# Performance work log

Measured on AMD Instinct MI355X. Metric: run time of the kernel, lower is better.

The kernel has to match this reference:

```python
import jax, jax.numpy as jnp
import numpy as np


def setup_inputs() -> dict:
    key = jax.random.key(0)
    B, DP, N = 4, 3, 8192
    positions = jax.random.normal(key, (B, DP, N), dtype=jnp.float32)
    return {"positions": positions, "k": 16}


def reference(positions, k):
    # positions: [B, Dp, N] ('simple' data_format)
    # Pairwise squared Euclidean distances between all N points per batch:
    # d2[b, i, j] = ||x_i - x_j||^2 = ||x_i||^2 + ||x_j||^2 - 2 x_i . x_j
    sq = jnp.sum(positions * positions, axis=1)                     # [B, N]
    dots = jnp.einsum('bdn,bdm->bnm', positions, positions)         # [B, N, N]
    d2 = sq[:, :, None] + sq[:, None, :] - 2.0 * dots               # [B, N, N]
    # k nearest neighbors (smallest distance; includes self at distance ~0)
    neg_d, idx = jax.lax.top_k(-d2, k)                              # [B, N, K]
    # Layer transposes raw op output [B, N, K] -> [B, K, N]
    NN = jnp.transpose(idx, (0, 2, 1)).astype(jnp.int32)            # [B, K, N]
    distances = jnp.transpose(-neg_d, (0, 2, 1))                    # [B, K, N]
    return (NN, distances)
```

## Files before the change

kernel.cpp:

```cpp
#include <hip/hip_runtime.h>
#include <stdint.h>

#define NPTS 8192
#define NPAIR 4096
#define NB 4
#define KNN 16
#define RQ 2
#define CCAP 20
#define DCAP 256
#define MARGIN 1.5e-3f

typedef unsigned long long u64;
typedef unsigned int u32;
typedef unsigned short u16;
typedef float f32x2 __attribute__((ext_vector_type(2)));

__device__ __forceinline__ u32 f2ord(float f) {
    u32 b = __float_as_uint(f);
    return (b & 0x80000000u) ? ~b : (b | 0x80000000u);
}
__device__ __forceinline__ float ord2f(u32 u) {
    u32 b = (u & 0x80000000u) ? (u & 0x7fffffffu) : ~u;
    return __uint_as_float(b);
}
__device__ __forceinline__ u64 shflx64(u64 v, int m) {
    u32 lo = (u32)v, hi = (u32)(v >> 32);
    lo = __shfl_xor(lo, m, 64);
    hi = __shfl_xor(hi, m, 64);
    return ((u64)hi << 32) | lo;
}

__global__ __launch_bounds__(256) void pack_kernel(const float* __restrict__ pos,
                                                   float4* __restrict__ pos8) {
    int t = blockIdx.x * 256 + threadIdx.x;
    int b = t >> 12;
    int m = t & (NPAIR - 1);
    const float* p = pos + (size_t)b * 3 * NPTS;
    float2 x = *(const float2*)&p[2 * m];
    float2 y = *(const float2*)&p[NPTS + 2 * m];
    float2 z = *(const float2*)&p[2 * NPTS + 2 * m];
    float s0 = __fadd_rn(__fadd_rn(__fmul_rn(x.x, x.x), __fmul_rn(y.x, y.x)), __fmul_rn(z.x, z.x));
    float s1 = __fadd_rn(__fadd_rn(__fmul_rn(x.y, x.y), __fmul_rn(y.y, y.y)), __fmul_rn(z.y, z.y));
    pos8[2 * t]     = make_float4(x.x, x.y, y.x, y.y);
    pos8[2 * t + 1] = make_float4(z.x, z.y, s0, s1);
}

#define RECOMP(r, idx, d2out)                                                           \
    { int _m = (int)(idx) >> 1, _h = (int)(idx) & 1;                                    \
      float4 _a = P8[2 * _m], _c = P8[2 * _m + 1];                                      \
      float _px = _h ? _a.y : _a.x, _py = _h ? _a.w : _a.z;                             \
      float _pz = _h ? _c.y : _c.x, _pw = _h ? _c.w : _c.z;                             \
      float _dot = __fmaf_rn(qz[r], _pz, __fmaf_rn(qy[r], _py, __fmul_rn(qx[r], _px))); \
      d2out = __fsub_rn(__fadd_rn(qw[r], _pw), __fmul_rn(2.0f, _dot)); }

#define PROC(Av, Cv, mm)                                                                \
    {                                                                                   \
        f32x2 x01 = {(Av).x, (Av).y}, y01 = {(Av).z, (Av).w};                           \
        f32x2 z01 = {(Cv).x, (Cv).y}, sq01 = {(Cv).z, (Cv).w};                          \
        _Pragma("unroll")                                                               \
        for (int r = 0; r < RQ; ++r) {                                                  \
            f32x2 dot01 = __builtin_elementwise_fma(                                    \
                qzv[r], z01, __builtin_elementwise_fma(qyv[r], y01, qxv[r] * x01));     \
            f32x2 val01 = __builtin_elementwise_fma(n2v, dot01, sq01);                  \
            if (val01.x < Tm[r]) { col[wv][r][c[r]][lane] = (u16)(2 * (mm));     c[r]++; } \
            if (val01.y < Tm[r]) { col[wv][r][c[r]][lane] = (u16)(2 * (mm) + 1); c[r]++; } \
        }                                                                               \
    }

#define TRIGC()                                                                         \
    {                                                                                   \
        if (__ballot(c[0] > 16)) tighten(0);                                            \
        if (__ballot(c[1] > 16)) tighten(1);                                            \
    }

__global__ __launch_bounds__(256) void knn_kernel(const float4* __restrict__ pos8,
                                                  float* __restrict__ out) {
    __shared__ u16 col[4][RQ][CCAP][64];
    __shared__ u16 dense[4][DCAP];
    const int lane = threadIdx.x & 63;
    const int wv = threadIdx.x >> 6;
    const int rowbase = blockIdx.x * (4 * RQ) + wv * RQ;
    const int b = rowbase >> 13;
    const int ib = rowbase & (NPTS - 1);
    const float4* __restrict__ P8 = pos8 + (size_t)b * NPAIR * 2;
    const u64 below = (1ull << lane) - 1ull;

    float qx[RQ], qy[RQ], qz[RQ], qw[RQ];
    {
        int m = ib >> 1;
        float4 a = P8[2 * m], cc = P8[2 * m + 1];
        qx[0] = a.x; qy[0] = a.z; qz[0] = cc.x; qw[0] = cc.z;
        qx[1] = a.y; qy[1] = a.w; qz[1] = cc.y; qw[1] = cc.w;
    }
    f32x2 qxv[RQ], qyv[RQ], qzv[RQ];
#pragma unroll
    for (int r = 0; r < RQ; ++r) {
        qxv[r] = (f32x2){qx[r], qx[r]};
        qyv[r] = (f32x2){qy[r], qy[r]};
        qzv[r] = (f32x2){qz[r], qz[r]};
    }
    const f32x2 n2v = {-2.0f, -2.0f};

    float Tm[RQ];
    int c[RQ];

    auto rank16f = [&](float v) -> float {
#pragma unroll
        for (int k = 2; k <= 64; k <<= 1)
#pragma unroll
            for (int j = k >> 1; j >= 1; j >>= 1) {
                float o = __shfl_xor(v, j, 64);
                bool up = ((lane & k) == 0) == ((lane & j) == 0);
                v = (up ? (v < o) : (v > o)) ? v : o;
            }
        return __shfl(v, 15, 64);
    };

    auto tighten = [&](int r) {
        u32 mn = 0xFFFFFFFFu;
#pragma unroll
        for (int t = 0; t < CCAP; ++t) {
            if (t < c[r]) {
                u32 idx = (u32)col[wv][r][t][lane];
                float d2; RECOMP(r, idx, d2);
                u32 o = f2ord(d2);
                mn = o < mn ? o : mn;
            }
        }
        u32 v = mn;
#pragma unroll
        for (int k = 2; k <= 64; k <<= 1)
#pragma unroll
            for (int j = k >> 1; j >= 1; j >>= 1) {
                u32 o = (u32)__shfl_xor((int)v, j, 64);
                bool up = ((lane & k) == 0) == ((lane & j) == 0);
                v = (up ? (v < o) : (v > o)) ? v : o;
            }
        u32 ordK = (u32)__shfl((int)v, 15, 64);
        int nc = 0;
#pragma unroll
        for (int t = 0; t < CCAP; ++t) {
            if (t < c[r]) {
                u32 idx = (u32)col[wv][r][t][lane];
                float d2; RECOMP(r, idx, d2);
                if (f2ord(d2) <= ordK) { col[wv][r][nc][lane] = (u16)idx; ++nc; }
            }
        }
        c[r] = nc;
#pragma unroll 1
        for (int it = 0; it < CCAP - 16; ++it) {
            if (c[r] > 16) {
                u64 mx = 0; int mt = 0;
#pragma unroll
                for (int t = 0; t < CCAP; ++t) {
                    if (t < c[r]) {
                        u32 idx = (u32)col[wv][r][t][lane];
                        float d2; RECOMP(r, idx, d2);
                        u64 key = ((u64)f2ord(d2) << 13) | idx;
                        if (key > mx) { mx = key; mt = t; }
                    }
                }
                col[wv][r][mt][lane] = col[wv][r][c[r] - 1][lane];
                c[r] -= 1;
            }
        }
        Tm[r] = fminf(Tm[r], (ord2f(ordK) - qw[r]) + MARGIN);
    };

    {
        float4 A[4], C[4];
#pragma unroll
        for (int s = 0; s < 4; ++s) {
            int m = s * 64 + lane;
            A[s] = P8[2 * m];
            C[s] = P8[2 * m + 1];
        }
#pragma unroll
        for (int r = 0; r < RQ; ++r) {
            f32x2 vv[4];
            float mn = __uint_as_float(0x7f800000u);
#pragma unroll
            for (int s = 0; s < 4; ++s) {
                f32x2 x01 = {A[s].x, A[s].y}, y01 = {A[s].z, A[s].w};
                f32x2 z01 = {C[s].x, C[s].y}, sq01 = {C[s].z, C[s].w};
                vv[s] = __builtin_elementwise_fma(
                    n2v, __builtin_elementwise_fma(qzv[r], z01,
                         __builtin_elementwise_fma(qyv[r], y01, qxv[r] * x01)), sq01);
                mn = fminf(mn, fminf(vv[s].x, vv[s].y));
            }
            float V16 = rank16f(mn);
            Tm[r] = V16 + 2.0f * MARGIN;
            c[r] = 0;
#pragma unroll
            for (int s = 0; s < 4; ++s) {
                int m = s * 64 + lane;
                if (vv[s].x < Tm[r]) { col[wv][r][c[r]][lane] = (u16)(2 * m);     c[r]++; }
                if (vv[s].y < Tm[r]) { col[wv][r][c[r]][lane] = (u16)(2 * m + 1); c[r]++; }
            }
        }
    }

#pragma unroll 1
    for (int g = 1; g < 16; ++g) {
        TRIGC();
        int base = g * 256;
        float4 A[4], C[4];
#pragma unroll
        for (int s = 0; s < 4; ++s) {
            int m = base + s * 64 + lane;
            A[s] = P8[2 * m];
            C[s] = P8[2 * m + 1];
        }
        PROC(A[0], C[0], base + lane);
        PROC(A[1], C[1], base + 64 + lane);
        TRIGC();
        PROC(A[2], C[2], base + 128 + lane);
        PROC(A[3], C[3], base + 192 + lane);
    }

#pragma unroll
    for (int r = 0; r < RQ; ++r) {
        int sum = c[r];
#pragma unroll
        for (int s2 = 1; s2 < 64; s2 <<= 1) sum += __shfl_xor(sum, s2, 64);
        if (sum > 64) tighten(r);
        int nc = 0;
#pragma unroll 1
        for (int t = 0; t < CCAP; ++t) {
            bool valid = t < c[r];
            u64 bal = __ballot(valid);
            if (!bal) break;
            if (valid) dense[wv][nc + (int)__popcll(bal & below)] = col[wv][r][t][lane];
            nc += (int)__popcll(bal);
        }
        u64 myk = ~0ULL;
        if (nc <= 64) {
            bool valid = lane < nc;
            u32 idx = valid ? (u32)dense[wv][lane] : 0u;
            float d2; RECOMP(r, idx, d2);
            u64 v = valid ? (((u64)f2ord(d2) << 13) | idx) : ~0ULL;
#pragma unroll
            for (int k = 2; k <= 64; k <<= 1)
#pragma unroll
                for (int j = k >> 1; j >= 1; j >>= 1) {
                    u64 o = shflx64(v, j);
                    bool up = ((lane & k) == 0) == ((lane & j) == 0);
                    v = (up ? (v < o) : (v > o)) ? v : o;
                }
            myk = v;
        } else {
            u64 s4[4];
#pragma unroll
            for (int t = 0; t < 4; ++t) {
                int bi = t * 64 + lane;
                bool valid = bi < nc;
                u32 idx = valid ? (u32)dense[wv][bi] : 0u;
                float d2; RECOMP(r, idx, d2);
                s4[t] = valid ? (((u64)f2ord(d2) << 13) | idx) : ~0ULL;
            }
#pragma unroll 1
            for (int rr = 0; rr < KNN; ++rr) {
                u64 lm = s4[0];
#pragma unroll
                for (int t = 1; t < 4; ++t) lm = s4[t] < lm ? s4[t] : lm;
                u64 mm = lm;
#pragma unroll
                for (int s2 = 1; s2 < 64; s2 <<= 1) { u64 o = shflx64(mm, s2); mm = o < mm ? o : mm; }
#pragma unroll
                for (int t = 0; t < 4; ++t) s4[t] = (s4[t] == mm) ? ~0ULL : s4[t];
                if (lane == rr) myk = mm;
            }
        }
        if (lane < KNN) {
            int iq = ib + r;
            size_t o1 = (size_t)(b * KNN + lane) * NPTS + iq;
            out[o1] = (float)(u32)(myk & (u64)(NPTS - 1));
            out[(size_t)NB * KNN * NPTS + o1] = ord2f((u32)(myk >> 13));
        }
    }
}

extern "C" void kernel_launch(void* const* d_in, const int* in_sizes, int n_in,
                              void* d_out, int out_size, void* d_ws, size_t ws_size,
                              hipStream_t stream) {
    const float* pos = (const float*)d_in[0];
    float* out = (float*)d_out;
    float4* pos8 = (float4*)d_ws;

    pack_kernel<<<dim3(NB * NPAIR / 256), dim3(256), 0, stream>>>(pos, pos8);
    knn_kernel<<<dim3(NB * NPTS / 8), dim3(256), 0, stream>>>(pos8, out);
}
```

Measured before the change: 184.1 us.

## Track candidate point pairs instead of single points with branchless append

Candidate lists now store the index of a point pair (the packed float4 pair) and admit a pair when the smaller of its two distances is under the threshold. Appends become branchless: the slot is always written and the counter increments conditionally. Tighten and the final selection recompute both distances of each pair, and the final sort thresholds are halved to match. This removes divergent branches in the hot scan loop, but each pair carries a possibly useless second point, so lists fill faster and tighten may run more often.

```diff
diff --git a/kernel.cpp b/kernel.cpp
--- a/kernel.cpp
+++ b/kernel.cpp
@@ -45,13 +45,12 @@
     pos8[2 * t + 1] = make_float4(z.x, z.y, s0, s1);
 }
 
-#define RECOMP(r, idx, d2out)                                                           \
-    { int _m = (int)(idx) >> 1, _h = (int)(idx) & 1;                                    \
-      float4 _a = P8[2 * _m], _c = P8[2 * _m + 1];                                      \
-      float _px = _h ? _a.y : _a.x, _py = _h ? _a.w : _a.z;                             \
-      float _pz = _h ? _c.y : _c.x, _pw = _h ? _c.w : _c.z;                             \
-      float _dot = __fmaf_rn(qz[r], _pz, __fmaf_rn(qy[r], _py, __fmul_rn(qx[r], _px))); \
-      d2out = __fsub_rn(__fadd_rn(qw[r], _pw), __fmul_rn(2.0f, _dot)); }
+#define RECOMP2(r, m, d0, d1)                                                           \
+    { float4 _a = P8[2 * (m)], _c = P8[2 * (m) + 1];                                    \
+      float _dot0 = __fmaf_rn(qz[r], _c.x, __fmaf_rn(qy[r], _a.z, __fmul_rn(qx[r], _a.x))); \
+      float _dot1 = __fmaf_rn(qz[r], _c.y, __fmaf_rn(qy[r], _a.w, __fmul_rn(qx[r], _a.y))); \
+      d0 = __fsub_rn(__fadd_rn(qw[r], _c.z), __fmul_rn(2.0f, _dot0));                   \
+      d1 = __fsub_rn(__fadd_rn(qw[r], _c.w), __fmul_rn(2.0f, _dot1)); }
 
 #define PROC(Av, Cv, mm)                                                                \
     {                                                                                   \
@@ -62,8 +61,8 @@
             f32x2 dot01 = __builtin_elementwise_fma(                                    \
                 qzv[r], z01, __builtin_elementwise_fma(qyv[r], y01, qxv[r] * x01));     \
             f32x2 val01 = __builtin_elementwise_fma(n2v, dot01, sq01);                  \
-            if (val01.x < Tm[r]) { col[wv][r][c[r]][lane] = (u16)(2 * (mm));     c[r]++; } \
-            if (val01.y < Tm[r]) { col[wv][r][c[r]][lane] = (u16)(2 * (mm) + 1); c[r]++; } \
+            col[wv][r][c[r]][lane] = (u16)(mm);                                         \
+            c[r] += (fminf(val01.x, val01.y) < Tm[r]) ? 1 : 0;                          \
         }                                                                               \
     }
 
@@ -121,10 +120,11 @@
 #pragma unroll
         for (int t = 0; t < CCAP; ++t) {
             if (t < c[r]) {
-                u32 idx = (u32)col[wv][r][t][lane];
-                float d2; RECOMP(r, idx, d2);
-                u32 o = f2ord(d2);
-                mn = o < mn ? o : mn;
+                u32 m = (u32)col[wv][r][t][lane];
+                float d0, d1; RECOMP2(r, m, d0, d1);
+                u32 om = f2ord(d0); u32 o1 = f2ord(d1);
+                om = o1 < om ? o1 : om;
+                mn = om < mn ? om : mn;
             }
         }
         u32 v = mn;
@@ -141,9 +141,11 @@
 #pragma unroll
         for (int t = 0; t < CCAP; ++t) {
             if (t < c[r]) {
-                u32 idx = (u32)col[wv][r][t][lane];
-                float d2; RECOMP(r, idx, d2);
-                if (f2ord(d2) <= ordK) { col[wv][r][nc][lane] = (u16)idx; ++nc; }
+                u32 m = (u32)col[wv][r][t][lane];
+                float d0, d1; RECOMP2(r, m, d0, d1);
+                u32 om = f2ord(d0); u32 o1 = f2ord(d1);
+                om = o1 < om ? o1 : om;
+                if (om <= ordK) { col[wv][r][nc][lane] = (u16)m; ++nc; }
             }
         }
         c[r] = nc;
@@ -154,9 +156,12 @@
 #pragma unroll
                 for (int t = 0; t < CCAP; ++t) {
                     if (t < c[r]) {
-                        u32 idx = (u32)col[wv][r][t][lane];
-                        float d2; RECOMP(r, idx, d2);
-                        u64 key = ((u64)f2ord(d2) << 13) | idx;
+                        u32 m = (u32)col[wv][r][t][lane];
+                        float d0, d1; RECOMP2(r, m, d0, d1);
+                        u32 o0 = f2ord(d0), o1 = f2ord(d1);
+                        u64 key = (o1 < o0)
+                            ? (((u64)o1 << 13) | (2 * m + 1))
+                            : (((u64)o0 << 13) | (2 * m));
                         if (key > mx) { mx = key; mt = t; }
                     }
                 }
@@ -194,8 +199,8 @@
 #pragma unroll
             for (int s = 0; s < 4; ++s) {
                 int m = s * 64 + lane;
-                if (vv[s].x < Tm[r]) { col[wv][r][c[r]][lane] = (u16)(2 * m);     c[r]++; }
-                if (vv[s].y < Tm[r]) { col[wv][r][c[r]][lane] = (u16)(2 * m + 1); c[r]++; }
+                col[wv][r][c[r]][lane] = (u16)m;
+                c[r] += (fminf(vv[s].x, vv[s].y) < Tm[r]) ? 1 : 0;
             }
         }
     }
@@ -223,7 +228,12 @@
         int sum = c[r];
 #pragma unroll
         for (int s2 = 1; s2 < 64; s2 <<= 1) sum += __shfl_xor(sum, s2, 64);
-        if (sum > 64) tighten(r);
+        if (sum > 32) {
+            tighten(r);
+            sum = c[r];
+#pragma unroll
+            for (int s2 = 1; s2 < 64; s2 <<= 1) sum += __shfl_xor(sum, s2, 64);
+        }
         int nc = 0;
 #pragma unroll 1
         for (int t = 0; t < CCAP; ++t) {
@@ -234,11 +244,12 @@
             nc += (int)__popcll(bal);
         }
         u64 myk = ~0ULL;
-        if (nc <= 64) {
-            bool valid = lane < nc;
-            u32 idx = valid ? (u32)dense[wv][lane] : 0u;
-            float d2; RECOMP(r, idx, d2);
-            u64 v = valid ? (((u64)f2ord(d2) << 13) | idx) : ~0ULL;
+        if (nc <= 32) {
+            bool valid = lane < 2 * nc;
+            u32 m = valid ? (u32)dense[wv][lane >> 1] : 0u;
+            float d0, d1; RECOMP2(r, m, d0, d1);
+            float dd = (lane & 1) ? d1 : d0;
+            u64 v = valid ? (((u64)f2ord(dd) << 13) | (2 * m + (lane & 1))) : ~0ULL;
 #pragma unroll
             for (int k = 2; k <= 64; k <<= 1)
 #pragma unroll
@@ -249,25 +260,26 @@
                 }
             myk = v;
         } else {
-            u64 s4[4];
+            u64 s8[8];
 #pragma unroll
             for (int t = 0; t < 4; ++t) {
                 int bi = t * 64 + lane;
                 bool valid = bi < nc;
-                u32 idx = valid ? (u32)dense[wv][bi] : 0u;
-                float d2; RECOMP(r, idx, d2);
-                s4[t] = valid ? (((u64)f2ord(d2) << 13) | idx) : ~0ULL;
+                u32 m = valid ? (u32)dense[wv][bi] : 0u;
+                float d0, d1; RECOMP2(r, m, d0, d1);
+                s8[2 * t]     = valid ? (((u64)f2ord(d0) << 13) | (2 * m))     : ~0ULL;
+                s8[2 * t + 1] = valid ? (((u64)f2ord(d1) << 13) | (2 * m + 1)) : ~0ULL;
             }
 #pragma unroll 1
             for (int rr = 0; rr < KNN; ++rr) {
-                u64 lm = s4[0];
-#pragma unroll
-                for (int t = 1; t < 4; ++t) lm = s4[t] < lm ? s4[t] : lm;
+                u64 lm = s8[0];
+#pragma unroll
+                for (int t = 1; t < 8; ++t) lm = s8[t] < lm ? s8[t] : lm;
                 u64 mm = lm;
 #pragma unroll
                 for (int s2 = 1; s2 < 64; s2 <<= 1) { u64 o = shflx64(mm, s2); mm = o < mm ? o : mm; }
 #pragma unroll
-                for (int t = 0; t < 4; ++t) s4[t] = (s4[t] == mm) ? ~0ULL : s4[t];
+                for (int t = 0; t < 8; ++t) s8[t] = (s8[t] == mm) ? ~0ULL : s8[t];
                 if (lane == rr) myk = mm;
             }
         }
```

Measured after the change: 165.6 us. 1.11x faster.
